# Optimization experiments

Measured on AMD Instinct MI355X. Metric: run time of the kernel, lower is better.

Reference implementation:

```python
import jax, jax.numpy as jnp
import numpy as np

EPS = 1e-5
NPOINT, K = 4096, 128
MLP = (64, 64, 128)
IN_CH = 3  # xyz only (Infea=0 -> use_feature=False)


def _conv_bn_relu(x, W, b, gamma, beta, mean, var):
    # 1x1 Conv2d == per-point channel GEMM: x [B,C,N,K], W [O,C]
    y = jnp.einsum('oc,bcnk->bonk', W, x) + b[None, :, None, None]
    inv = gamma / jnp.sqrt(var + EPS)
    y = y * inv[None, :, None, None] + (beta - mean * inv)[None, :, None, None]
    return jax.nn.relu(y)


def setup_inputs() -> dict:
    key = jax.random.key(0)
    ks = jax.random.split(key, 8)
    inp = {
        'grouped_pc': jax.random.normal(ks[0], (1, IN_CH, NPOINT, K), dtype=jnp.float32),
        'valid': (jax.random.uniform(ks[1], (1, 1, NPOINT, K)) > 0.3).astype(jnp.float32),
    }
    c_prev = IN_CH
    for i, c_out in enumerate(MLP, start=1):
        kw = jax.random.fold_in(ks[2], i)
        fan_in = c_prev  # kaiming_normal for 1x1 conv
        inp[f'W{i}'] = jax.random.normal(kw, (c_out, c_prev), dtype=jnp.float32) * np.sqrt(2.0 / fan_in)
        inp[f'b{i}'] = jnp.zeros((c_out,), dtype=jnp.float32)
        inp[f'gamma{i}'] = jnp.ones((c_out,), dtype=jnp.float32)
        inp[f'beta{i}'] = jnp.zeros((c_out,), dtype=jnp.float32)
        inp[f'mean{i}'] = jax.random.normal(jax.random.fold_in(ks[3], i), (c_out,), dtype=jnp.float32) * 0.1
        inp[f'var{i}'] = jax.random.uniform(jax.random.fold_in(ks[4], i), (c_out,), minval=0.5, maxval=1.5).astype(jnp.float32)
        c_prev = c_out
    return inp


def reference(grouped_pc, valid,
              W1, b1, gamma1, beta1, mean1, var1,
              W2, b2, gamma2, beta2, mean2, var2,
              W3, b3, gamma3, beta3, mean3, var3):
    x = _conv_bn_relu(grouped_pc, W1, b1, gamma1, beta1, mean1, var1)
    x = _conv_bn_relu(x, W2, b2, gamma2, beta2, mean2, var2)
    x = _conv_bn_relu(x, W3, b3, gamma3, beta3, mean3, var3)
    return x * valid  # validity mask broadcast over channels
```

## Files before the change

kernel.cpp:

```cpp
#include <hip/hip_runtime.h>
#include <math.h>

#define EPS 1e-5f
#define NPK (4096 * 128)

typedef __attribute__((ext_vector_type(8))) short bf16x8;
typedef __attribute__((ext_vector_type(4))) short short4v;
typedef __attribute__((ext_vector_type(4))) float f32x4;

__device__ __forceinline__ short f2bf(float f) {
    union { float f; unsigned u; } x; x.f = f;
    unsigned r = x.u + 0x7fffu + ((x.u >> 16) & 1u);
    return (short)(r >> 16);
}

#define WS_A1 0
#define WS_C1 192
#define WS_C2 256
#define WS_C3 320
#define WS_BF 448

__global__ void prep_kernel(
    const float* __restrict__ W1, const float* __restrict__ b1,
    const float* __restrict__ g1, const float* __restrict__ be1,
    const float* __restrict__ m1, const float* __restrict__ v1,
    const float* __restrict__ W2, const float* __restrict__ b2,
    const float* __restrict__ g2, const float* __restrict__ be2,
    const float* __restrict__ m2, const float* __restrict__ v2,
    const float* __restrict__ W3, const float* __restrict__ b3,
    const float* __restrict__ g3, const float* __restrict__ be3,
    const float* __restrict__ m3, const float* __restrict__ v3,
    float* __restrict__ ws)
{
    const int t = threadIdx.x;
    if (t < 64) {
        float inv1 = g1[t] * rsqrtf(v1[t] + EPS);
        ws[WS_C1 + t] = b1[t] * inv1 + be1[t] - m1[t] * inv1;
        ws[WS_A1 + t * 3 + 0] = W1[t * 3 + 0] * inv1;
        ws[WS_A1 + t * 3 + 1] = W1[t * 3 + 1] * inv1;
        ws[WS_A1 + t * 3 + 2] = W1[t * 3 + 2] * inv1;
        float inv2 = g2[t] * rsqrtf(v2[t] + EPS);
        ws[WS_C2 + t] = b2[t] * inv2 + be2[t] - m2[t] * inv2;
    }
    if (t < 128) {
        float inv3 = g3[t] * rsqrtf(v3[t] + EPS);
        ws[WS_C3 + t] = b3[t] * inv3 + be3[t] - m3[t] * inv3;
    }
    short* A2b = (short*)(ws + WS_BF);
    short* A3b = A2b + 64 * 64;
    for (int idx = t; idx < 64 * 64; idx += 256) {
        int o = idx >> 6;
        float inv = g2[o] * rsqrtf(v2[o] + EPS);
        A2b[idx] = f2bf(W2[idx] * inv);
    }
    for (int idx = t; idx < 128 * 64; idx += 256) {
        int o = idx >> 6;
        float inv = g3[o] * rsqrtf(v3[o] + EPS);
        A3b[idx] = f2bf(W3[idx] * inv);
    }
}

__global__ __launch_bounds__(256) void pointnet_mfma(
    const float* __restrict__ x, const float* __restrict__ valid,
    const float* __restrict__ ws, float* __restrict__ out)
{
    __shared__ short h1[128 * 72];
    __shared__ short h2[128 * 72];
    __shared__ float vld[128];

    const int t = threadIdx.x;
    const int pbase = blockIdx.x * 128;

    const float* __restrict__ A1 = ws + WS_A1;
    const float* __restrict__ C1 = ws + WS_C1;
    const float* __restrict__ C2 = ws + WS_C2;
    const float* __restrict__ C3 = ws + WS_C3;
    const short* __restrict__ A2b = (const short*)(ws + WS_BF);
    const short* __restrict__ A3b = A2b + 64 * 64;

    {
        const int pl = t & 127;
        const int half = t >> 7;
        const int pg = pbase + pl;
        const float x0 = x[pg];
        const float x1 = x[pg + NPK];
        const float x2 = x[pg + 2 * NPK];
        if (half == 0) vld[pl] = valid[pg];
        const int cb = half * 32;
#pragma unroll
        for (int g = 0; g < 4; ++g) {
            bf16x8 vb;
#pragma unroll
            for (int j = 0; j < 8; ++j) {
                const int ch = cb + g * 8 + j;
                float a = C1[ch];
                a = fmaf(A1[ch * 3 + 0], x0, a);
                a = fmaf(A1[ch * 3 + 1], x1, a);
                a = fmaf(A1[ch * 3 + 2], x2, a);
                vb[j] = f2bf(fmaxf(a, 0.0f));
            }
            *(bf16x8*)&h1[pl * 72 + cb + g * 8] = vb;
        }
    }
    __syncthreads();

    const int lane = t & 63;
    const int w = t >> 6;
    const int lanelo = lane & 15;
    const int quad = lane >> 4;

    bf16x8 a2f[2], a3f[2][2];
#pragma unroll
    for (int ks = 0; ks < 2; ++ks)
        a2f[ks] = *(const bf16x8*)&A2b[(w * 16 + lanelo) * 64 + ks * 32 + quad * 8];
#pragma unroll
    for (int mt = 0; mt < 2; ++mt)
#pragma unroll
        for (int ks = 0; ks < 2; ++ks)
            a3f[mt][ks] = *(const bf16x8*)&A3b[((w * 2 + mt) * 16 + lanelo) * 64 + ks * 32 + quad * 8];

    const f32x4 bias2 = *(const f32x4*)&C2[w * 16 + quad * 4];
#pragma unroll
    for (int nt = 0; nt < 8; ++nt) {
        const int n = nt * 16 + lanelo;
        bf16x8 b0 = *(const bf16x8*)&h1[n * 72 + 0  + quad * 8];
        bf16x8 b1 = *(const bf16x8*)&h1[n * 72 + 32 + quad * 8];
        f32x4 acc = {0.f, 0.f, 0.f, 0.f};
        acc = __builtin_amdgcn_mfma_f32_16x16x32_bf16(a2f[0], b0, acc, 0, 0, 0);
        acc = __builtin_amdgcn_mfma_f32_16x16x32_bf16(a2f[1], b1, acc, 0, 0, 0);
        short4v o;
#pragma unroll
        for (int r = 0; r < 4; ++r)
            o[r] = f2bf(fmaxf(acc[r] + bias2[r], 0.0f));
        *(short4v*)&h2[n * 72 + w * 16 + quad * 4] = o;
    }
    __syncthreads();

    f32x4 acc3[16];
#pragma unroll
    for (int i = 0; i < 16; ++i) acc3[i] = (f32x4){0.f, 0.f, 0.f, 0.f};
#pragma unroll
    for (int nt = 0; nt < 8; ++nt) {
        const int n = nt * 16 + lanelo;
        bf16x8 b0 = *(const bf16x8*)&h2[n * 72 + 0  + quad * 8];
        bf16x8 b1 = *(const bf16x8*)&h2[n * 72 + 32 + quad * 8];
#pragma unroll
        for (int mt = 0; mt < 2; ++mt) {
            acc3[mt * 8 + nt] = __builtin_amdgcn_mfma_f32_16x16x32_bf16(a3f[mt][0], b0, acc3[mt * 8 + nt], 0, 0, 0);
            acc3[mt * 8 + nt] = __builtin_amdgcn_mfma_f32_16x16x32_bf16(a3f[mt][1], b1, acc3[mt * 8 + nt], 0, 0, 0);
        }
    }

#pragma unroll
    for (int mt = 0; mt < 2; ++mt) {
        const int mrow = (w * 2 + mt) * 16 + quad * 4;
        const f32x4 bias3 = *(const f32x4*)&C3[mrow];
#pragma unroll
        for (int nt = 0; nt < 8; ++nt) {
            const float v = vld[nt * 16 + lanelo];
            const int pg = pbase + nt * 16 + lanelo;
            const f32x4 a = acc3[mt * 8 + nt];
#pragma unroll
            for (int r = 0; r < 4; ++r)
                out[(mrow + r) * NPK + pg] = fmaxf(a[r] + bias3[r], 0.0f) * v;
        }
    }
}

extern "C" void kernel_launch(void* const* d_in, const int* in_sizes, int n_in,
                              void* d_out, int out_size, void* d_ws, size_t ws_size,
                              hipStream_t stream) {
    const float* x     = (const float*)d_in[0];
    const float* valid = (const float*)d_in[1];

    const float* W1 = (const float*)d_in[2];
    const float* b1 = (const float*)d_in[3];
    const float* g1 = (const float*)d_in[4];
    const float* be1 = (const float*)d_in[5];
    const float* m1 = (const float*)d_in[6];
    const float* v1 = (const float*)d_in[7];

    const float* W2 = (const float*)d_in[8];
    const float* b2 = (const float*)d_in[9];
    const float* g2 = (const float*)d_in[10];
    const float* be2 = (const float*)d_in[11];
    const float* m2 = (const float*)d_in[12];
    const float* v2 = (const float*)d_in[13];

    const float* W3 = (const float*)d_in[14];
    const float* b3 = (const float*)d_in[15];
    const float* g3 = (const float*)d_in[16];
    const float* be3 = (const float*)d_in[17];
    const float* m3 = (const float*)d_in[18];
    const float* v3 = (const float*)d_in[19];

    float* ws  = (float*)d_ws;
    float* out = (float*)d_out;

    prep_kernel<<<1, 256, 0, stream>>>(W1, b1, g1, be1, m1, v1,
                                       W2, b2, g2, be2, m2, v2,
                                       W3, b3, g3, be3, m3, v3, ws);

    pointnet_mfma<<<NPK / 128, 256, 0, stream>>>(x, valid, ws, out);
}
```

Measured before the change: 358.8 us.

## Swap MFMA operand roles so outputs are point-contiguous and store 16-byte nontemporal vectors

```diff
diff --git a/kernel.cpp b/kernel.cpp
--- a/kernel.cpp
+++ b/kernel.cpp
@@ -5,7 +5,6 @@
 #define NPK (4096 * 128)
 
 typedef __attribute__((ext_vector_type(8))) short bf16x8;
-typedef __attribute__((ext_vector_type(4))) short short4v;
 typedef __attribute__((ext_vector_type(4))) float f32x4;
 
 __device__ __forceinline__ short f2bf(float f) {
@@ -46,17 +45,23 @@
         float inv3 = g3[t] * rsqrtf(v3[t] + EPS);
         ws[WS_C3 + t] = b3[t] * inv3 + be3[t] - m3[t] * inv3;
     }
-    short* A2b = (short*)(ws + WS_BF);
-    short* A3b = A2b + 64 * 64;
+    short* W2f = (short*)(ws + WS_BF);
+    short* W3f = W2f + 64 * 64;
     for (int idx = t; idx < 64 * 64; idx += 256) {
-        int o = idx >> 6;
+        int j = idx & 7, lane = (idx >> 3) & 63, tile = idx >> 9;
+        int nt = tile >> 1, ks = tile & 1;
+        int o = nt * 16 + (lane & 15);
+        int i = ks * 32 + (lane >> 4) * 8 + j;
         float inv = g2[o] * rsqrtf(v2[o] + EPS);
-        A2b[idx] = f2bf(W2[idx] * inv);
+        W2f[idx] = f2bf(W2[o * 64 + i] * inv);
     }
     for (int idx = t; idx < 128 * 64; idx += 256) {
-        int o = idx >> 6;
+        int j = idx & 7, lane = (idx >> 3) & 63, tile = idx >> 9;
+        int nt = tile >> 1, ks = tile & 1;
+        int o = nt * 16 + (lane & 15);
+        int i = ks * 32 + (lane >> 4) * 8 + j;
         float inv = g3[o] * rsqrtf(v3[o] + EPS);
-        A3b[idx] = f2bf(W3[idx] * inv);
+        W3f[idx] = f2bf(W3[o * 64 + i] * inv);
     }
 }
 
@@ -64,31 +69,31 @@
     const float* __restrict__ x, const float* __restrict__ valid,
     const float* __restrict__ ws, float* __restrict__ out)
 {
-    __shared__ short h1[128 * 72];
-    __shared__ short h2[128 * 72];
-    __shared__ float vld[128];
+    __shared__ short h1[64 * 72];
+    __shared__ short h2[64 * 72];
+    __shared__ float vld[64];
 
     const int t = threadIdx.x;
-    const int pbase = blockIdx.x * 128;
+    const int pbase = blockIdx.x * 64;
 
     const float* __restrict__ A1 = ws + WS_A1;
     const float* __restrict__ C1 = ws + WS_C1;
     const float* __restrict__ C2 = ws + WS_C2;
     const float* __restrict__ C3 = ws + WS_C3;
-    const short* __restrict__ A2b = (const short*)(ws + WS_BF);
-    const short* __restrict__ A3b = A2b + 64 * 64;
+    const short* __restrict__ W2f = (const short*)(ws + WS_BF);
+    const short* __restrict__ W3f = W2f + 64 * 64;
 
     {
-        const int pl = t & 127;
-        const int half = t >> 7;
+        const int pl = t & 63;
+        const int half = t >> 6;
         const int pg = pbase + pl;
         const float x0 = x[pg];
         const float x1 = x[pg + NPK];
         const float x2 = x[pg + 2 * NPK];
         if (half == 0) vld[pl] = valid[pg];
-        const int cb = half * 32;
+        const int cb = half * 16;
 #pragma unroll
-        for (int g = 0; g < 4; ++g) {
+        for (int g = 0; g < 2; ++g) {
             bf16x8 vb;
 #pragma unroll
             for (int j = 0; j < 8; ++j) {
@@ -109,60 +114,43 @@
     const int lanelo = lane & 15;
     const int quad = lane >> 4;
 
-    bf16x8 a2f[2], a3f[2][2];
+    {
+        bf16x8 a0 = *(const bf16x8*)&h1[(w * 16 + lanelo) * 72 + 0  + quad * 8];
+        bf16x8 a1 = *(const bf16x8*)&h1[(w * 16 + lanelo) * 72 + 32 + quad * 8];
 #pragma unroll
-    for (int ks = 0; ks < 2; ++ks)
-        a2f[ks] = *(const bf16x8*)&A2b[(w * 16 + lanelo) * 64 + ks * 32 + quad * 8];
+        for (int nt = 0; nt < 4; ++nt) {
+            bf16x8 b0 = *(const bf16x8*)&W2f[((nt * 2 + 0) * 64 + lane) * 8];
+            bf16x8 b1 = *(const bf16x8*)&W2f[((nt * 2 + 1) * 64 + lane) * 8];
+            f32x4 acc = {0.f, 0.f, 0.f, 0.f};
+            acc = __builtin_amdgcn_mfma_f32_16x16x32_bf16(a0, b0, acc, 0, 0, 0);
+            acc = __builtin_amdgcn_mfma_f32_16x16x32_bf16(a1, b1, acc, 0, 0, 0);
+            const float bias = C2[nt * 16 + lanelo];
 #pragma unroll
-    for (int mt = 0; mt < 2; ++mt)
-#pragma unroll
-        for (int ks = 0; ks < 2; ++ks)
-            a3f[mt][ks] = *(const bf16x8*)&A3b[((w * 2 + mt) * 16 + lanelo) * 64 + ks * 32 + quad * 8];
-
-    const f32x4 bias2 = *(const f32x4*)&C2[w * 16 + quad * 4];
-#pragma unroll
-    for (int nt = 0; nt < 8; ++nt) {
-        const int n = nt * 16 + lanelo;
-        bf16x8 b0 = *(const bf16x8*)&h1[n * 72 + 0  + quad * 8];
-        bf16x8 b1 = *(const bf16x8*)&h1[n * 72 + 32 + quad * 8];
-        f32x4 acc = {0.f, 0.f, 0.f, 0.f};
-        acc = __builtin_amdgcn_mfma_f32_16x16x32_bf16(a2f[0], b0, acc, 0, 0, 0);
-        acc = __builtin_amdgcn_mfma_f32_16x16x32_bf16(a2f[1], b1, acc, 0, 0, 0);
-        short4v o;
-#pragma unroll
-        for (int r = 0; r < 4; ++r)
-            o[r] = f2bf(fmaxf(acc[r] + bias2[r], 0.0f));
-        *(short4v*)&h2[n * 72 + w * 16 + quad * 4] = o;
+            for (int r = 0; r < 4; ++r)
+                h2[(w * 16 + quad * 4 + r) * 72 + nt * 16 + lanelo] =
+                    f2bf(fmaxf(acc[r] + bias, 0.0f));
+        }
     }
     __syncthreads();
 
-    f32x4 acc3[16];
-#pragma unroll
-    for (int i = 0; i < 16; ++i) acc3[i] = (f32x4){0.f, 0.f, 0.f, 0.f};
-#pragma unroll
-    for (int nt = 0; nt < 8; ++nt) {
-        const int n = nt * 16 + lanelo;
-        bf16x8 b0 = *(const bf16x8*)&h2[n * 72 + 0  + quad * 8];
-        bf16x8 b1 = *(const bf16x8*)&h2[n * 72 + 32 + quad * 8];
-#pragma unroll
-        for (int mt = 0; mt < 2; ++mt) {
-            acc3[mt * 8 + nt] = __builtin_amdgcn_mfma_f32_16x16x32_bf16(a3f[mt][0], b0, acc3[mt * 8 + nt], 0, 0, 0);
-            acc3[mt * 8 + nt] = __builtin_amdgcn_mfma_f32_16x16x32_bf16(a3f[mt][1], b1, acc3[mt * 8 + nt], 0, 0, 0);
-        }
-    }
-
-#pragma unroll
-    for (int mt = 0; mt < 2; ++mt) {
-        const int mrow = (w * 2 + mt) * 16 + quad * 4;
-        const f32x4 bias3 = *(const f32x4*)&C3[mrow];
+    {
+        bf16x8 a0 = *(const bf16x8*)&h2[(w * 16 + lanelo) * 72 + 0  + quad * 8];
+        bf16x8 a1 = *(const bf16x8*)&h2[(w * 16 + lanelo) * 72 + 32 + quad * 8];
+        const f32x4 v4 = *(const f32x4*)&vld[w * 16 + quad * 4];
+        const int pstore = pbase + w * 16 + quad * 4;
 #pragma unroll
         for (int nt = 0; nt < 8; ++nt) {
-            const float v = vld[nt * 16 + lanelo];
-            const int pg = pbase + nt * 16 + lanelo;
-            const f32x4 a = acc3[mt * 8 + nt];
+            bf16x8 b0 = *(const bf16x8*)&W3f[((nt * 2 + 0) * 64 + lane) * 8];
+            bf16x8 b1 = *(const bf16x8*)&W3f[((nt * 2 + 1) * 64 + lane) * 8];
+            f32x4 acc = {0.f, 0.f, 0.f, 0.f};
+            acc = __builtin_amdgcn_mfma_f32_16x16x32_bf16(a0, b0, acc, 0, 0, 0);
+            acc = __builtin_amdgcn_mfma_f32_16x16x32_bf16(a1, b1, acc, 0, 0, 0);
+            const float bias = C3[nt * 16 + lanelo];
+            f32x4 o;
 #pragma unroll
             for (int r = 0; r < 4; ++r)
-                out[(mrow + r) * NPK + pg] = fmaxf(a[r] + bias3[r], 0.0f) * v;
+                o[r] = fmaxf(acc[r] + bias, 0.0f) * v4[r];
+            __builtin_nontemporal_store(o, (f32x4*)&out[(nt * 16 + lanelo) * NPK + pstore]);
         }
     }
 }
@@ -201,5 +189,5 @@
                                        W2, b2, g2, be2, m2, v2,
                                        W3, b3, g3, be3, m3, v3, ws);
 
-    pointnet_mfma<<<NPK / 128, 256, 0, stream>>>(x, valid, ws, out);
+    pointnet_mfma<<<NPK / 64, 256, 0, stream>>>(x, valid, ws, out);
 }
```

After: 389.7 us. +8.6%, slower.
